# Kernel tuning notes

Hardware: AMD Instinct MI355X
Metric: run time of the kernel (lower is better)

Reference implementation:

```python
import jax, jax.numpy as jnp
import numpy as np

HEADS = 8
KV_HEADS = 4
HEAD_DIM = 256
HIDDEN = 2560
WINDOW = 1024          # sliding_window (layer is sliding: (0+1) % 6 != 0)
SCALE = 256.0 ** -0.5  # query_pre_attn_scalar ** -0.5
ROPE_BASE = 10000.0    # rope_local_base_freq for sliding layers
EPS = 1e-6
NEG = -1e30


def rms_norm(x, w, eps=EPS):
    # x: [..., D]; effective weight is (1 + param) per the RMSNorm module
    var = jnp.mean(x * x, axis=-1, keepdims=True)
    return x * jax.lax.rsqrt(var + eps) * w


def rope(x, base, offset):
    # x: [B, H, T, D]; rotate-half RoPE over the full head_dim
    T, D = x.shape[2], x.shape[3]
    half = D // 2
    pos = (offset + jnp.arange(T)).astype(jnp.float32)           # [T]
    inv_freq = base ** (-jnp.arange(half, dtype=jnp.float32) * 2.0 / D)  # [half]
    ang = pos[:, None] * inv_freq[None, :]                       # [T, half]
    cos, sin = jnp.cos(ang), jnp.sin(ang)
    x1, x2 = x[..., :half], x[..., half:]
    return jnp.concatenate([x1 * cos - x2 * sin, x2 * cos + x1 * sin], axis=-1)


def setup_inputs() -> dict:
    key = jax.random.key(0)
    ks = jax.random.split(key, 7)
    B, T, S = 2, 1024, 4096
    w_std = 0.02
    return {
        "x": jax.random.normal(ks[0], (B, T, HIDDEN), dtype=jnp.float32),
        "k_cache": jax.random.normal(ks[1], (B, KV_HEADS, S, HEAD_DIM), dtype=jnp.float32),
        "v_cache": jax.random.normal(ks[2], (B, KV_HEADS, S, HEAD_DIM), dtype=jnp.float32),
        "wq": jax.random.normal(ks[3], (HIDDEN, HEADS * HEAD_DIM), dtype=jnp.float32) * w_std,
        "wk": jax.random.normal(ks[4], (HIDDEN, KV_HEADS * HEAD_DIM), dtype=jnp.float32) * w_std,
        "wv": jax.random.normal(ks[5], (HIDDEN, KV_HEADS * HEAD_DIM), dtype=jnp.float32) * w_std,
        "wo": jax.random.normal(ks[6], (HEADS * HEAD_DIM, HIDDEN), dtype=jnp.float32) * w_std,
        "q_norm_w": jnp.zeros((HEAD_DIM,), dtype=jnp.float32),
        "k_norm_w": jnp.zeros((HEAD_DIM,), dtype=jnp.float32),
        "pos_offset": 2048,
        "cache_index": 2048,
    }


def reference(x, k_cache, v_cache, wq, wk, wv, wo, q_norm_w, k_norm_w, pos_offset, cache_index):
    B, T, _ = x.shape
    # QKV projections -> [B, H, T, D]
    q = (x @ wq).reshape(B, T, HEADS, HEAD_DIM).transpose(0, 2, 1, 3)
    k = (x @ wk).reshape(B, T, KV_HEADS, HEAD_DIM).transpose(0, 2, 1, 3)
    v = (x @ wv).reshape(B, T, KV_HEADS, HEAD_DIM).transpose(0, 2, 1, 3)
    # per-head RMSNorm (effective weight 1 + param)
    q = rms_norm(q, 1.0 + q_norm_w)
    k = rms_norm(k, 1.0 + k_norm_w)
    # RoPE with position offset
    q = rope(q, ROPE_BASE, pos_offset)
    k = rope(k, ROPE_BASE, pos_offset)
    # KV cache update at cache_index along the sequence axis
    k_new = jax.lax.dynamic_update_slice(k_cache, k, (0, 0, cache_index, 0))
    v_new = jax.lax.dynamic_update_slice(v_cache, v, (0, 0, cache_index, 0))
    S = k_new.shape[2]
    # sliding-window validity mask over cached keys (as in the module: shared over queries)
    idx = jnp.arange(S)
    valid = (idx < cache_index + T) & (idx >= cache_index + T - WINDOW)   # [S]
    # GQA attention: group queries over kv heads
    G = HEADS // KV_HEADS
    qg = q.reshape(B, KV_HEADS, G, T, HEAD_DIM)
    scores = jnp.einsum('bkgtd,bksd->bkgts', qg, k_new) * SCALE           # [B,KV,G,T,S]
    scores = jnp.where(valid[None, None, None, None, :], scores, NEG)
    p = jax.nn.softmax(scores, axis=-1)
    out = jnp.einsum('bkgts,bksd->bkgtd', p, v_new)                       # [B,KV,G,T,D]
    out = out.reshape(B, HEADS, T, HEAD_DIM).transpose(0, 2, 1, 3).reshape(B, T, HEADS * HEAD_DIM)
    return out @ wo, k_new, v_new
```

## Files before the change

kernel.cpp:

```cpp
#include <hip/hip_runtime.h>

typedef __bf16 bf16;
typedef __bf16 bf16x8 __attribute__((ext_vector_type(8)));
typedef __bf16 bf16x4 __attribute__((ext_vector_type(4)));
typedef float f32x4 __attribute__((ext_vector_type(4)));

#define MFMA16(a, b, c) __builtin_amdgcn_mfma_f32_16x16x32_bf16(a, b, c, 0, 0, 0)

__global__ __launch_bounds__(256) void cvt_x_kernel(const float* __restrict__ x,
                                                    bf16* __restrict__ xb) {
  const long i = (long)blockIdx.x * 256 + threadIdx.x;
  const float4 v = ((const float4*)x)[i];
  bf16x4 o4;
  o4.x = (bf16)v.x; o4.y = (bf16)v.y; o4.z = (bf16)v.z; o4.w = (bf16)v.w;
  ((bf16x4*)xb)[i] = o4;
}

__global__ __launch_bounds__(256) void wqkv_trans_kernel(const float* __restrict__ wq,
                                                         const float* __restrict__ wk,
                                                         const float* __restrict__ wv,
                                                         bf16* __restrict__ dst) {
  __shared__ float tile[32][33];
  const int k0 = blockIdx.x * 32, n0 = blockIdx.y * 32;
  const float* src; int col, srcN;
  if (n0 < 2048)      { src = wq; col = n0;        srcN = 2048; }
  else if (n0 < 3072) { src = wk; col = n0 - 2048; srcN = 1024; }
  else                { src = wv; col = n0 - 3072; srcN = 1024; }
  const int tx = threadIdx.x, ty = threadIdx.y;
#pragma unroll
  for (int i = 0; i < 4; ++i)
    tile[ty + i * 8][tx] = src[(long)(k0 + ty + i * 8) * srcN + col + tx];
  __syncthreads();
#pragma unroll
  for (int i = 0; i < 4; ++i)
    dst[(long)(n0 + ty + i * 8) * 2560 + k0 + tx] = (bf16)tile[tx][ty + i * 8];
}

__global__ __launch_bounds__(256) void wo_trans_kernel(const float* __restrict__ wo,
                                                       bf16* __restrict__ dst) {
  __shared__ float tile[32][33];
  const int k0 = blockIdx.x * 32, n0 = blockIdx.y * 32;
  const int tx = threadIdx.x, ty = threadIdx.y;
#pragma unroll
  for (int i = 0; i < 4; ++i)
    tile[ty + i * 8][tx] = wo[(long)(k0 + ty + i * 8) * 2560 + n0 + tx];
  __syncthreads();
#pragma unroll
  for (int i = 0; i < 4; ++i)
    dst[(long)(n0 + ty + i * 8) * 2048 + k0 + tx] = (bf16)tile[tx][ty + i * 8];
}

__global__ __launch_bounds__(256) void v_trans_kernel(const float* __restrict__ vout,
                                                      const int* __restrict__ p_ci,
                                                      bf16* __restrict__ vt) {
  __shared__ float tile[32][33];
  const int s0 = blockIdx.x * 32, d0 = blockIdx.y * 32, bk = blockIdx.z;
  const int ci = *p_ci;
  const int tx = threadIdx.x, ty = threadIdx.y;
  const float* src = vout + ((long)bk * 4096 + ci) * 256;
#pragma unroll
  for (int i = 0; i < 4; ++i)
    tile[ty + i * 8][tx] = src[(long)(s0 + ty + i * 8) * 256 + d0 + tx];
  __syncthreads();
  bf16* dstb = vt + ((long)bk * 256 + d0) * 1024 + s0;
#pragma unroll
  for (int i = 0; i < 4; ++i)
    dstb[(long)(ty + i * 8) * 1024 + tx] = (bf16)tile[tx][ty + i * 8];
}

template <int K, int N>
__global__ __launch_bounds__(256) void gemm_kernel(const bf16* __restrict__ A,
                                                   const bf16* __restrict__ BT,
                                                   float* __restrict__ C) {
  __shared__ bf16 As[128 * 40];
  __shared__ bf16 Bs[128 * 40];
  const int bm = blockIdx.x, bn = blockIdx.y;
  const int tid = threadIdx.x;
  const int wave = tid >> 6, lane = tid & 63;
  const int quad = lane >> 4, l16 = lane & 15;
  const int wm = (wave & 1) * 64, wn = (wave >> 1) * 64;
  f32x4 acc[4][4] = {};
  const int r0 = tid >> 2, o0 = (tid & 3) * 8;
  const int r1 = r0 + 64;
  const bf16* Ag = A + (long)(bm * 128) * K;
  const bf16* Bg = BT + (long)(bn * 128) * K;
  for (int k0 = 0; k0 < K; k0 += 32) {
    uint4 a0 = *(const uint4*)(Ag + (long)r0 * K + k0 + o0);
    uint4 a1 = *(const uint4*)(Ag + (long)r1 * K + k0 + o0);
    uint4 b0 = *(const uint4*)(Bg + (long)r0 * K + k0 + o0);
    uint4 b1 = *(const uint4*)(Bg + (long)r1 * K + k0 + o0);
    __syncthreads();
    *(uint4*)(As + r0 * 40 + o0) = a0;
    *(uint4*)(As + r1 * 40 + o0) = a1;
    *(uint4*)(Bs + r0 * 40 + o0) = b0;
    *(uint4*)(Bs + r1 * 40 + o0) = b1;
    __syncthreads();
    bf16x8 af[4], bfr[4];
#pragma unroll
    for (int mi = 0; mi < 4; ++mi)
      af[mi] = *(const bf16x8*)(As + (wm + mi * 16 + l16) * 40 + quad * 8);
#pragma unroll
    for (int ni = 0; ni < 4; ++ni)
      bfr[ni] = *(const bf16x8*)(Bs + (wn + ni * 16 + l16) * 40 + quad * 8);
#pragma unroll
    for (int mi = 0; mi < 4; ++mi)
#pragma unroll
      for (int ni = 0; ni < 4; ++ni)
        acc[mi][ni] = MFMA16(af[mi], bfr[ni], acc[mi][ni]);
  }
  const int crow = bm * 128 + wm + quad * 4;
  const int ccol = bn * 128 + wn + l16;
#pragma unroll
  for (int mi = 0; mi < 4; ++mi)
#pragma unroll
    for (int ni = 0; ni < 4; ++ni)
#pragma unroll
      for (int r = 0; r < 4; ++r)
        C[(long)(crow + mi * 16 + r) * N + ccol + ni * 16] = acc[mi][ni][r];
}

__global__ __launch_bounds__(256) void normrope_kernel(
    const float* __restrict__ qkv, const float* __restrict__ qw,
    const float* __restrict__ kw, const int* __restrict__ p_pos,
    const int* __restrict__ p_ci, float* __restrict__ kout,
    float* __restrict__ vout, bf16* __restrict__ q_bf, bf16* __restrict__ k_bf) {
  const int bt = blockIdx.x, slot = blockIdx.y;
  const int t = bt & 1023, b = bt >> 10;
  const int d = threadIdx.x;
  const float val = qkv[(long)bt * 4096 + slot * 256 + d];
  const int ci = *p_ci;
  if (slot >= 12) {
    vout[((long)(b * 4 + (slot - 12)) * 4096 + ci + t) * 256 + d] = val;
    return;
  }
  __shared__ float red[4];
  __shared__ float rowbuf[256];
  float ss = val * val;
#pragma unroll
  for (int i = 1; i < 64; i <<= 1) ss += __shfl_xor(ss, i);
  if ((d & 63) == 0) red[d >> 6] = ss;
  __syncthreads();
  const float tot = red[0] + red[1] + red[2] + red[3];
  const float rstd = rsqrtf(tot * (1.0f / 256.0f) + 1e-6f);
  const bool isq = slot < 8;
  const float wv = isq ? qw[d] : kw[d];
  const float nv = val * rstd * (1.0f + wv);
  rowbuf[d] = nv;
  __syncthreads();
  const int e = d & 127;
  const float inv_freq = exp2f((float)e * -0.10381025296522976f);
  const float ang = (float)(*p_pos + t) * inv_freq;
  float sn, cs;
  sincosf(ang, &sn, &cs);
  float outv;
  if (d < 128) outv = nv * cs - rowbuf[d + 128] * sn;
  else         outv = nv * cs + rowbuf[d - 128] * sn;
  if (isq) {
    q_bf[((long)(b * 8 + slot) * 1024 + t) * 256 + d] = (bf16)outv;
  } else {
    const int kh = slot - 8;
    kout[((long)(b * 4 + kh) * 4096 + ci + t) * 256 + d] = outv;
    k_bf[((long)(b * 4 + kh) * 1024 + t) * 256 + d] = (bf16)outv;
  }
}

__global__ __launch_bounds__(256) void attn_kernel(const bf16* __restrict__ q_bf,
                                                   const bf16* __restrict__ k_bf,
                                                   const bf16* __restrict__ vt_bf,
                                                   bf16* __restrict__ attn) {
  __shared__ bf16 Ks[64 * 264];
  __shared__ bf16 Vs[256 * 72];
  __shared__ bf16 Ps[64 * 72];
  const int qt = blockIdx.x, h = blockIdx.y, b = blockIdx.z;
  const int kvh = h >> 1;
  const int tid = threadIdx.x;
  const int wave = tid >> 6, lane = tid & 63, quad = lane >> 4, l16 = lane & 15;
  bf16x8 qf[8];
  const bf16* qg =
      q_bf + ((long)(b * 8 + h) * 1024 + qt * 64 + wave * 16 + l16) * 256 + quad * 8;
#pragma unroll
  for (int i = 0; i < 8; ++i) qf[i] = *(const bf16x8*)(qg + i * 32);
  f32x4 o[16] = {};
  float m_r[4] = {-1e30f, -1e30f, -1e30f, -1e30f};
  float l_r[4] = {0.f, 0.f, 0.f, 0.f};
  const float sfac = 0.0625f * 1.44269504088896f;
  const bf16* kgb = k_bf + (long)(b * 4 + kvh) * 1024 * 256;
  const bf16* vgb = vt_bf + (long)(b * 4 + kvh) * 256 * 1024;
  for (int st = 0; st < 16; ++st) {
    __syncthreads();
#pragma unroll
    for (int i = 0; i < 8; ++i) {
      int c = tid + i * 256;
      *(uint4*)(Ks + (c >> 5) * 264 + (c & 31) * 8) =
          *(const uint4*)(kgb + (long)(st * 64 + (c >> 5)) * 256 + (c & 31) * 8);
    }
#pragma unroll
    for (int i = 0; i < 8; ++i) {
      int c = tid + i * 256;
      *(uint4*)(Vs + (c >> 3) * 72 + (c & 7) * 8) =
          *(const uint4*)(vgb + (long)(c >> 3) * 1024 + st * 64 + (c & 7) * 8);
    }
    __syncthreads();
    f32x4 sacc[4] = {};
#pragma unroll
    for (int kk = 0; kk < 8; ++kk) {
#pragma unroll
      for (int ni = 0; ni < 4; ++ni) {
        bf16x8 kf = *(const bf16x8*)(Ks + (ni * 16 + l16) * 264 + kk * 32 + quad * 8);
        sacc[ni] = MFMA16(qf[kk], kf, sacc[ni]);
      }
    }
    float alpha_r[4];
#pragma unroll
    for (int r = 0; r < 4; ++r) {
      float s0 = sacc[0][r] * sfac, s1 = sacc[1][r] * sfac;
      float s2 = sacc[2][r] * sfac, s3 = sacc[3][r] * sfac;
      float mx = fmaxf(fmaxf(s0, s1), fmaxf(s2, s3));
#pragma unroll
      for (int dd = 1; dd < 16; dd <<= 1) mx = fmaxf(mx, __shfl_xor(mx, dd));
      float mnew = fmaxf(m_r[r], mx);
      float al = exp2f(m_r[r] - mnew);
      m_r[r] = mnew;
      alpha_r[r] = al;
      float p0 = exp2f(s0 - mnew), p1 = exp2f(s1 - mnew);
      float p2 = exp2f(s2 - mnew), p3 = exp2f(s3 - mnew);
      float rs = p0 + p1 + p2 + p3;
#pragma unroll
      for (int dd = 1; dd < 16; dd <<= 1) rs += __shfl_xor(rs, dd);
      l_r[r] = l_r[r] * al + rs;
      const int prow = (wave * 16 + quad * 4 + r) * 72;
      Ps[prow + l16] = (bf16)p0;
      Ps[prow + 16 + l16] = (bf16)p1;
      Ps[prow + 32 + l16] = (bf16)p2;
      Ps[prow + 48 + l16] = (bf16)p3;
    }
#pragma unroll
    for (int n2 = 0; n2 < 16; ++n2) {
      f32x4 tv = o[n2];
      tv.x *= alpha_r[0]; tv.y *= alpha_r[1]; tv.z *= alpha_r[2]; tv.w *= alpha_r[3];
      o[n2] = tv;
    }
    __syncthreads();
    bf16x8 pf0 = *(const bf16x8*)(Ps + (wave * 16 + l16) * 72 + quad * 8);
    bf16x8 pf1 = *(const bf16x8*)(Ps + (wave * 16 + l16) * 72 + 32 + quad * 8);
#pragma unroll
    for (int n2 = 0; n2 < 16; ++n2) {
      bf16x8 vf0 = *(const bf16x8*)(Vs + (n2 * 16 + l16) * 72 + quad * 8);
      o[n2] = MFMA16(pf0, vf0, o[n2]);
      bf16x8 vf1 = *(const bf16x8*)(Vs + (n2 * 16 + l16) * 72 + 32 + quad * 8);
      o[n2] = MFMA16(pf1, vf1, o[n2]);
    }
  }
  float inv_l[4];
#pragma unroll
  for (int r = 0; r < 4; ++r) inv_l[r] = 1.0f / l_r[r];
  bf16* og = attn + ((long)(b * 1024 + qt * 64 + wave * 16 + quad * 4)) * 2048 +
             h * 256 + l16;
#pragma unroll
  for (int n2 = 0; n2 < 16; ++n2)
#pragma unroll
    for (int r = 0; r < 4; ++r)
      og[(long)r * 2048 + n2 * 16] = (bf16)(o[n2][r] * inv_l[r]);
}

extern "C" void kernel_launch(void* const* d_in, const int* in_sizes, int n_in,
                              void* d_out, int out_size, void* d_ws, size_t ws_size,
                              hipStream_t stream) {
  const float* x = (const float*)d_in[0];
  const float* k_cache = (const float*)d_in[1];
  const float* v_cache = (const float*)d_in[2];
  const float* wq = (const float*)d_in[3];
  const float* wk = (const float*)d_in[4];
  const float* wv = (const float*)d_in[5];
  const float* wo = (const float*)d_in[6];
  const float* qnw = (const float*)d_in[7];
  const float* knw = (const float*)d_in[8];
  const int* p_pos = (const int*)d_in[9];
  const int* p_ci = (const int*)d_in[10];

  float* out0 = (float*)d_out;
  float* kout = out0 + (long)2 * 1024 * 2560;
  float* vout = kout + (long)2 * 4 * 4096 * 256;

  char* w = (char*)d_ws;
  bf16* x_bf = (bf16*)(w);
  bf16* wqkv_t = (bf16*)(w + 10485760);
  bf16* wo_t = (bf16*)(w + 31457280);
  float* qkv = (float*)(w + 41943040);
  bf16* q_bf = (bf16*)(w + 75497472);
  bf16* k_bf = (bf16*)(w + 83886080);
  bf16* vt_bf = (bf16*)(w + 88080384);
  bf16* attn_b = (bf16*)(w + 92274688);

  hipMemcpyAsync(kout, k_cache, (size_t)8388608 * 4, hipMemcpyDeviceToDevice, stream);
  hipMemcpyAsync(vout, v_cache, (size_t)8388608 * 4, hipMemcpyDeviceToDevice, stream);

  cvt_x_kernel<<<5120, 256, 0, stream>>>(x, x_bf);
  dim3 tb(32, 8);
  wqkv_trans_kernel<<<dim3(80, 128), tb, 0, stream>>>(wq, wk, wv, wqkv_t);
  wo_trans_kernel<<<dim3(64, 80), tb, 0, stream>>>(wo, wo_t);

  gemm_kernel<2560, 4096><<<dim3(16, 32), 256, 0, stream>>>(x_bf, wqkv_t, qkv);

  normrope_kernel<<<dim3(2048, 16), 256, 0, stream>>>(qkv, qnw, knw, p_pos, p_ci,
                                                      kout, vout, q_bf, k_bf);

  v_trans_kernel<<<dim3(32, 8, 8), tb, 0, stream>>>(vout, p_ci, vt_bf);

  attn_kernel<<<dim3(16, 8, 2), 256, 0, stream>>>(q_bf, k_bf, vt_bf, attn_b);

  gemm_kernel<2048, 2560><<<dim3(16, 20), 256, 0, stream>>>(attn_b, wo_t, out0);
}
```

Baseline: 426.5 us.

## Load GEMM and attention tiles directly into LDS with swizzled layouts

Replaces the register-staged global-to-shared copies in the GEMM and attention kernels with direct global_load_lds (16-byte) transfers. Because those writes land contiguously per wave, padded LDS rows are dropped and XOR/rotation swizzles are applied to the global source addresses and the fragment reads to avoid bank conflicts. The aim is to cut VGPR use and instruction count on the load path and free LDS. The risk is address-math overhead and correctness of the swizzle mapping.

```diff
diff --git a/kernel.cpp b/kernel.cpp
--- a/kernel.cpp
+++ b/kernel.cpp
@@ -6,6 +6,11 @@
 typedef float f32x4 __attribute__((ext_vector_type(4)));
 
 #define MFMA16(a, b, c) __builtin_amdgcn_mfma_f32_16x16x32_bf16(a, b, c, 0, 0, 0)
+
+#define GLL(lds, g)                                                    \
+  __builtin_amdgcn_global_load_lds(                                    \
+      (const __attribute__((address_space(1))) void*)(g),              \
+      (__attribute__((address_space(3))) void*)(lds), 16, 0, 0)
 
 __global__ __launch_bounds__(256) void cvt_x_kernel(const float* __restrict__ x,
                                                     bf16* __restrict__ xb) {
@@ -72,36 +77,42 @@
 __global__ __launch_bounds__(256) void gemm_kernel(const bf16* __restrict__ A,
                                                    const bf16* __restrict__ BT,
                                                    float* __restrict__ C) {
-  __shared__ bf16 As[128 * 40];
-  __shared__ bf16 Bs[128 * 40];
+  __shared__ bf16 As[128 * 32];
+  __shared__ bf16 Bs[128 * 32];
   const int bm = blockIdx.x, bn = blockIdx.y;
   const int tid = threadIdx.x;
   const int wave = tid >> 6, lane = tid & 63;
   const int quad = lane >> 4, l16 = lane & 15;
   const int wm = (wave & 1) * 64, wn = (wave >> 1) * 64;
   f32x4 acc[4][4] = {};
-  const int r0 = tid >> 2, o0 = (tid & 3) * 8;
+  const int r0 = tid >> 2;
+  const int cc0 = ((tid & 3) - (r0 >> 1)) & 3;
   const int r1 = r0 + 64;
+  const int cc1 = ((tid & 3) - (r1 >> 1)) & 3;
   const bf16* Ag = A + (long)(bm * 128) * K;
   const bf16* Bg = BT + (long)(bn * 128) * K;
+  bf16* AsW  = As + wave * 512;
+  bf16* AsW2 = As + 2048 + wave * 512;
+  bf16* BsW  = Bs + wave * 512;
+  bf16* BsW2 = Bs + 2048 + wave * 512;
   for (int k0 = 0; k0 < K; k0 += 32) {
-    uint4 a0 = *(const uint4*)(Ag + (long)r0 * K + k0 + o0);
-    uint4 a1 = *(const uint4*)(Ag + (long)r1 * K + k0 + o0);
-    uint4 b0 = *(const uint4*)(Bg + (long)r0 * K + k0 + o0);
-    uint4 b1 = *(const uint4*)(Bg + (long)r1 * K + k0 + o0);
-    __syncthreads();
-    *(uint4*)(As + r0 * 40 + o0) = a0;
-    *(uint4*)(As + r1 * 40 + o0) = a1;
-    *(uint4*)(Bs + r0 * 40 + o0) = b0;
-    *(uint4*)(Bs + r1 * 40 + o0) = b1;
+    __syncthreads();
+    GLL(AsW, Ag + (long)r0 * K + k0 + cc0 * 8);
+    GLL(AsW2, Ag + (long)r1 * K + k0 + cc1 * 8);
+    GLL(BsW, Bg + (long)r0 * K + k0 + cc0 * 8);
+    GLL(BsW2, Bg + (long)r1 * K + k0 + cc1 * 8);
     __syncthreads();
     bf16x8 af[4], bfr[4];
 #pragma unroll
-    for (int mi = 0; mi < 4; ++mi)
-      af[mi] = *(const bf16x8*)(As + (wm + mi * 16 + l16) * 40 + quad * 8);
-#pragma unroll
-    for (int ni = 0; ni < 4; ++ni)
-      bfr[ni] = *(const bf16x8*)(Bs + (wn + ni * 16 + l16) * 40 + quad * 8);
+    for (int mi = 0; mi < 4; ++mi) {
+      const int r = wm + mi * 16 + l16;
+      af[mi] = *(const bf16x8*)(As + r * 32 + (((quad + (r >> 1)) & 3) * 8));
+    }
+#pragma unroll
+    for (int ni = 0; ni < 4; ++ni) {
+      const int r = wn + ni * 16 + l16;
+      bfr[ni] = *(const bf16x8*)(Bs + r * 32 + (((quad + (r >> 1)) & 3) * 8));
+    }
 #pragma unroll
     for (int mi = 0; mi < 4; ++mi)
 #pragma unroll
@@ -168,8 +179,8 @@
                                                    const bf16* __restrict__ k_bf,
                                                    const bf16* __restrict__ vt_bf,
                                                    bf16* __restrict__ attn) {
-  __shared__ bf16 Ks[64 * 264];
-  __shared__ bf16 Vs[256 * 72];
+  __shared__ bf16 Ks[64 * 256];
+  __shared__ bf16 Vs[256 * 64];
   __shared__ bf16 Ps[64 * 72];
   const int qt = blockIdx.x, h = blockIdx.y, b = blockIdx.z;
   const int kvh = h >> 1;
@@ -186,19 +197,21 @@
   const float sfac = 0.0625f * 1.44269504088896f;
   const bf16* kgb = k_bf + (long)(b * 4 + kvh) * 1024 * 256;
   const bf16* vgb = vt_bf + (long)(b * 4 + kvh) * 256 * 1024;
+  const int krow = tid >> 5, kccp = tid & 31;
+  const int kcc = kccp ^ (krow & 7);
+  const int vrow0 = tid >> 3, vccp = tid & 7;
   for (int st = 0; st < 16; ++st) {
     __syncthreads();
 #pragma unroll
     for (int i = 0; i < 8; ++i) {
-      int c = tid + i * 256;
-      *(uint4*)(Ks + (c >> 5) * 264 + (c & 31) * 8) =
-          *(const uint4*)(kgb + (long)(st * 64 + (c >> 5)) * 256 + (c & 31) * 8);
+      GLL(Ks + (i * 256 + wave * 64) * 8,
+          kgb + (long)(st * 64 + krow + i * 8) * 256 + kcc * 8);
     }
 #pragma unroll
     for (int i = 0; i < 8; ++i) {
-      int c = tid + i * 256;
-      *(uint4*)(Vs + (c >> 3) * 72 + (c & 7) * 8) =
-          *(const uint4*)(vgb + (long)(c >> 3) * 1024 + st * 64 + (c & 7) * 8);
+      const int vr = vrow0 + i * 32;
+      GLL(Vs + (i * 256 + wave * 64) * 8,
+          vgb + (long)vr * 1024 + st * 64 + (vccp ^ (vr & 7)) * 8);
     }
     __syncthreads();
     f32x4 sacc[4] = {};
@@ -206,7 +219,8 @@
     for (int kk = 0; kk < 8; ++kk) {
 #pragma unroll
       for (int ni = 0; ni < 4; ++ni) {
-        bf16x8 kf = *(const bf16x8*)(Ks + (ni * 16 + l16) * 264 + kk * 32 + quad * 8);
+        const int r = ni * 16 + l16;
+        bf16x8 kf = *(const bf16x8*)(Ks + r * 256 + (((kk * 4 + quad) ^ (r & 7)) * 8));
         sacc[ni] = MFMA16(qf[kk], kf, sacc[ni]);
       }
     }
@@ -245,9 +259,10 @@
     bf16x8 pf1 = *(const bf16x8*)(Ps + (wave * 16 + l16) * 72 + 32 + quad * 8);
 #pragma unroll
     for (int n2 = 0; n2 < 16; ++n2) {
-      bf16x8 vf0 = *(const bf16x8*)(Vs + (n2 * 16 + l16) * 72 + quad * 8);
+      const int r = n2 * 16 + l16;
+      bf16x8 vf0 = *(const bf16x8*)(Vs + r * 64 + ((quad ^ (r & 7)) * 8));
       o[n2] = MFMA16(pf0, vf0, o[n2]);
-      bf16x8 vf1 = *(const bf16x8*)(Vs + (n2 * 16 + l16) * 72 + 32 + quad * 8);
+      bf16x8 vf1 = *(const bf16x8*)(Vs + r * 64 + (((4 + quad) ^ (r & 7)) * 8));
       o[n2] = MFMA16(pf1, vf1, o[n2]);
     }
   }
```

After: 420.6 us. No clear change (-1.4%).
